# Performance work log

Measured on AMD Instinct MI355X. Metric: run time of the kernel, lower is better.

## Reference

```python
import jax, jax.numpy as jnp
import numpy as np

N = 64
D_MODEL = 512
L_MAX = 2048
BATCH = 8
DT_MIN, DT_MAX = 1e-3, 1e-1


def _make_s4_buffers(n):
    r = np.arange(1, n + 1, dtype=np.float64)
    # hippo[i,j] = sqrt(2(i+1)+1)*sqrt(2(j+1)+1) if i>j, (i+1)+1 on diag, else 0
    hippo = np.where(r[:, None] > r[None, :],
                     np.sqrt(2 * r[:, None] + 1.0) * np.sqrt(2 * r[None, :] + 1.0),
                     0.0)
    hippo = hippo + np.diag(r + 1.0)
    nhippo = -hippo
    p = 0.5 * np.sqrt(2.0 * r + 1.0)
    q = 2.0 * p
    S = nhippo + p[:, None] * q[None, :]
    lmbda, V = np.linalg.eig(S)
    Vc = V.conj().T
    p = Vc @ p
    q = Vc @ q.conj()
    return (p.astype(np.complex64), q.astype(np.complex64), lmbda.astype(np.complex64))


def setup_inputs() -> dict:
    key = jax.random.key(0)
    ku, kb, kc, ks = jax.random.split(key, 4)
    u = jax.random.normal(ku, (BATCH, L_MAX, D_MODEL), dtype=jnp.float32)
    std = float(np.sqrt(2.0 / (N + D_MODEL)))  # xavier_normal for (n, d_model)
    B = jax.random.normal(kb, (D_MODEL, N), dtype=jnp.float32) * std
    Ct = jax.random.normal(kc, (D_MODEL, N), dtype=jnp.float32) * std
    D = jnp.ones((D_MODEL,), dtype=jnp.float32)
    scale = float(np.log(DT_MAX) - np.log(DT_MIN))
    log_step = jax.random.uniform(ks, (D_MODEL,), dtype=jnp.float32) * scale + float(np.log(DT_MIN))
    p, q, lmbda = _make_s4_buffers(N)
    omega_l = np.exp(2j * np.pi / L_MAX * np.arange(L_MAX)).astype(np.complex64)
    return {"u": u, "B": B, "Ct": Ct, "D": D, "log_step": log_step,
            "p": jnp.asarray(p), "q": jnp.asarray(q), "lmbda": jnp.asarray(lmbda),
            "omega_l": jnp.asarray(omega_l)}


def _s4_kernel(B, Ct, log_step, p, q, lmbda, omega_l):
    L = omega_l.shape[0]
    step = jnp.exp(log_step)                                   # [d]
    g = jnp.outer(2.0 / step, (1.0 - omega_l) / (1.0 + omega_l))  # [d, L] complex
    c = 2.0 / (1.0 + omega_l)                                  # [L]
    # shared Cauchy resolvent: 1/(g - lambda), [d, L, n]
    r = 1.0 / (g[:, :, None] - lmbda)
    a0 = jnp.conj(Ct)  # [d, n]
    a1 = jnp.conj(q)   # [n]
    k00 = jnp.einsum('dn,dln->dl', a0 * B, r)
    k01 = jnp.einsum('dn,dln->dl', a0 * p, r)
    k10 = jnp.einsum('dn,dln->dl', a1 * B, r)
    k11 = jnp.einsum('n,dln->dl', a1 * p, r)
    at_roots = c * (k00 - k01 * (1.0 / (1.0 + k11)) * k10)     # [d, L]
    Kf = jnp.fft.ifft(at_roots, n=L, axis=-1)
    order = (-jnp.arange(L)) % L                               # [0, L-1, ..., 1]
    return Kf[:, order].real                                   # [d, L] float32


def reference(u, B, Ct, D, log_step, p, q, lmbda, omega_l):
    L = u.shape[1]
    K = _s4_kernel(B, Ct, log_step, p, q, lmbda, omega_l)      # [d, L]
    # non-circular FFT convolution
    ud = jnp.fft.rfft(jnp.pad(u, ((0, 0), (0, L), (0, 0))), axis=1)   # [B, L+1, d]
    Kd = jnp.fft.rfft(jnp.pad(K, ((0, 0), (0, L))), axis=-1)          # [d, L+1]
    y = jnp.fft.irfft(ud.transpose(0, 2, 1) * Kd, axis=-1)[..., :L]   # [B, d, L]
    return y.transpose(0, 2, 1) + D[None, None, :] * u
```

## Files before the change

### kernel.cpp

```cpp
#include <hip/hip_runtime.h>
#include <hip/hip_bf16.h>

#define NT 256
#define R2f 0.70710678118654752f
#define CS1 0.92387953251128674f
#define SN1 0.38268343236508978f
#define PI2 6.2831853071795865f

__device__ __forceinline__ float2 cmulf(float2 a, float2 b) {
    return make_float2(a.x * b.x - a.y * b.y, a.x * b.y + a.y * b.x);
}
__device__ __forceinline__ float2 cadd(float2 a, float2 b) { return make_float2(a.x + b.x, a.y + b.y); }
__device__ __forceinline__ float2 csub(float2 a, float2 b) { return make_float2(a.x - b.x, a.y - b.y); }

template<bool INV>
__device__ __forceinline__ float2 tww(float2 v, float wx, float wy) {
    float sy = INV ? -wy : wy;
    return make_float2(v.x * wx - v.y * sy, v.x * sy + v.y * wx);
}
template<bool INV>
__device__ __forceinline__ float2 mul_mi(float2 v) {
    return INV ? make_float2(-v.y, v.x) : make_float2(v.y, -v.x);
}

template<bool INV>
__device__ __forceinline__ void dft4(float2& a, float2& b, float2& c, float2& d) {
    float2 t0 = cadd(a, c), t1 = csub(a, c);
    float2 t2 = cadd(b, d), t3 = csub(b, d);
    float2 jt3 = mul_mi<INV>(t3);
    a = cadd(t0, t2);
    c = csub(t0, t2);
    b = cadd(t1, jt3);
    d = csub(t1, jt3);
}

template<bool INV>
__device__ __forceinline__ void fft16_tail(float2 v[16]) {
    v[5]  = tww<INV>(v[5],  CS1, -SN1);
    v[9]  = tww<INV>(v[9],  R2f, -R2f);
    v[13] = tww<INV>(v[13], SN1, -CS1);
    v[6]  = tww<INV>(v[6],  R2f, -R2f);
    v[10] = mul_mi<INV>(v[10]);
    v[14] = tww<INV>(v[14], -R2f, -R2f);
    v[7]  = tww<INV>(v[7],  SN1, -CS1);
    v[11] = tww<INV>(v[11], -R2f, -R2f);
    v[15] = tww<INV>(v[15], -CS1,  SN1);
    dft4<INV>(v[0],  v[1],  v[2],  v[3]);
    dft4<INV>(v[4],  v[5],  v[6],  v[7]);
    dft4<INV>(v[8],  v[9],  v[10], v[11]);
    dft4<INV>(v[12], v[13], v[14], v[15]);
    float2 t;
    t = v[1];  v[1]  = v[4];  v[4]  = t;
    t = v[2];  v[2]  = v[8];  v[8]  = t;
    t = v[3];  v[3]  = v[12]; v[12] = t;
    t = v[6];  v[6]  = v[9];  v[9]  = t;
    t = v[7];  v[7]  = v[13]; v[13] = t;
    t = v[11]; v[11] = v[14]; v[14] = t;
}

template<bool INV>
__device__ __forceinline__ void fft16(float2 v[16]) {
    dft4<INV>(v[0], v[4], v[8],  v[12]);
    dft4<INV>(v[1], v[5], v[9],  v[13]);
    dft4<INV>(v[2], v[6], v[10], v[14]);
    dft4<INV>(v[3], v[7], v[11], v[15]);
    fft16_tail<INV>(v);
}

__device__ __forceinline__ void fft16_hz(float2 v[16]) {
    #pragma unroll
    for (int i = 0; i < 4; ++i) {
        float2 a = v[i], b = v[i + 4];
        float2 jb = make_float2(b.y, -b.x);
        v[i]      = cadd(a, b);
        v[i + 4]  = cadd(a, jb);
        v[i + 8]  = csub(a, b);
        v[i + 12] = csub(a, jb);
    }
    fft16_tail<false>(v);
}

template<bool INV>
__device__ __forceinline__ void twchain(float2 v[16], float ang) {
    float s, c;
    __sincosf(INV ? ang : -ang, &s, &c);
    float2 w = make_float2(c, s);
    float2 t = w;
    v[1] = cmulf(v[1], t);
    #pragma unroll
    for (int a = 2; a < 16; ++a) { t = cmulf(t, w); v[a] = cmulf(v[a], t); }
}

template<bool INV>
__device__ void fft4096(float2 v[16], float2* lds, int tid) {
    const int hi = tid >> 4, lo = tid & 15;
    if (!INV) {
        fft16_hz(v);
        twchain<false>(v, PI2 * (float)tid * (1.0f / 4096.0f));
        __syncthreads();
        #pragma unroll
        for (int a = 0; a < 16; ++a) lds[tid + 256 * a] = v[a];
        __syncthreads();
        #pragma unroll
        for (int m1 = 0; m1 < 16; ++m1) v[m1] = lds[(m1 * 16 + lo) + 256 * hi];
        fft16<false>(v);
        twchain<false>(v, PI2 * (float)lo * (1.0f / 256.0f));
        __syncthreads();
        #pragma unroll
        for (int b = 0; b < 16; ++b) { int e = lo + 16 * b + 256 * hi; lds[e ^ b] = v[b]; }
        __syncthreads();
        #pragma unroll
        for (int m0 = 0; m0 < 16; ++m0) { int e = m0 + 16 * lo + 256 * hi; v[m0] = lds[e ^ lo]; }
        fft16<false>(v);
    } else {
        fft16<true>(v);
        __syncthreads();
        #pragma unroll
        for (int m0 = 0; m0 < 16; ++m0) { int e = m0 + 16 * lo + 256 * hi; lds[e ^ lo] = v[m0]; }
        __syncthreads();
        #pragma unroll
        for (int b = 0; b < 16; ++b) { int e = lo + 16 * b + 256 * hi; v[b] = lds[e ^ b]; }
        twchain<true>(v, PI2 * (float)lo * (1.0f / 256.0f));
        fft16<true>(v);
        __syncthreads();
        #pragma unroll
        for (int m1 = 0; m1 < 16; ++m1) lds[(m1 * 16 + lo) + 256 * hi] = v[m1];
        __syncthreads();
        #pragma unroll
        for (int a = 0; a < 16; ++a) v[a] = lds[tid + 256 * a];
        twchain<true>(v, PI2 * (float)tid * (1.0f / 4096.0f));
        fft16<true>(v);
    }
}

__global__ __launch_bounds__(256) void cauchy_kernel(
    const float* __restrict__ Bmat, const float* __restrict__ Ct,
    const float* __restrict__ log_step,
    const float2* __restrict__ p, const float2* __restrict__ q,
    const float2* __restrict__ lmbda, const float2* __restrict__ omega,
    float2* __restrict__ at)
{
    __shared__ float4 wA[64];
    __shared__ float4 wB[64];
    const int tid = threadIdx.x;
    const int d = blockIdx.x >> 1;
    const int lbase = (blockIdx.x & 1) << 9;

    if (tid < 64) {
        float b  = Bmat[d * 64 + tid];
        float ct = Ct[d * 64 + tid];
        float2 pp = p[tid], qq = q[tid];
        float2 lam = lmbda[tid];
        wA[tid] = make_float4(lam.x, lam.y, ct * b, qq.x * pp.x + qq.y * pp.y);
        wB[tid] = make_float4(ct * pp.x, ct * pp.y, b * qq.x, b * qq.y);
    }
    __syncthreads();

    const float two_over_dt = 2.0f * __expf(-log_step[d]);
    float2* atd = at + ((size_t)d << 11);

    float gx[2], gy[2], ccx[2], ccy[2];
    float S00x[2], S00y[2], Sax[2], Say[2], Sbx[2], Sby[2];
    float Scx[2], Scy[2], Sdx[2], Sdy[2], S11x[2], S11y[2];

    #pragma unroll
    for (int il = 0; il < 2; ++il) {
        int l = lbase + tid + 256 * il;
        float2 om = omega[l];
        float dnx = 1.0f + om.x, dny = om.y;
        float id2 = __builtin_amdgcn_rcpf(dnx * dnx + dny * dny);
        float ivx = dnx * id2, ivy = -dny * id2;
        ccx[il] = 2.0f * ivx; ccy[il] = 2.0f * ivy;
        float nmx = 1.0f - om.x, nmy = -om.y;
        gx[il] = two_over_dt * (nmx * ivx - nmy * ivy);
        gy[il] = two_over_dt * (nmx * ivy + nmy * ivx);
        S00x[il] = 0.f; S00y[il] = 0.f; Sax[il] = 0.f; Say[il] = 0.f;
        Sbx[il] = 0.f; Sby[il] = 0.f; Scx[il] = 0.f; Scy[il] = 0.f;
        Sdx[il] = 0.f; Sdy[il] = 0.f; S11x[il] = 0.f; S11y[il] = 0.f;
    }

    #pragma unroll 4
    for (int n = 0; n < 64; ++n) {
        float4 A  = wA[n];
        float4 Bw = wB[n];
        #pragma unroll
        for (int il = 0; il < 2; ++il) {
            float dx  = gx[il] - A.x;
            float dy  = gy[il] - A.y;
            float ir  = __builtin_amdgcn_rcpf(fmaf(dx, dx, dy * dy));
            float rx  = dx * ir;
            float ry  = -dy * ir;
            S00x[il] = fmaf(A.z,  rx, S00x[il]); S00y[il] = fmaf(A.z,  ry, S00y[il]);
            S11x[il] = fmaf(A.w,  rx, S11x[il]); S11y[il] = fmaf(A.w,  ry, S11y[il]);
            Sax[il]  = fmaf(Bw.x, rx, Sax[il]);  Say[il]  = fmaf(Bw.x, ry, Say[il]);
            Sbx[il]  = fmaf(Bw.y, rx, Sbx[il]);  Sby[il]  = fmaf(Bw.y, ry, Sby[il]);
            Scx[il]  = fmaf(Bw.z, rx, Scx[il]);  Scy[il]  = fmaf(Bw.z, ry, Scy[il]);
            Sdx[il]  = fmaf(Bw.w, rx, Sdx[il]);  Sdy[il]  = fmaf(Bw.w, ry, Sdy[il]);
        }
    }

    #pragma unroll
    for (int il = 0; il < 2; ++il) {
        float k01x = Sax[il] - Sby[il], k01y = Say[il] + Sbx[il];
        float k10x = Scx[il] + Sdy[il], k10y = Scy[il] - Sdx[il];
        float ntx = k01x * k10x - k01y * k10y;
        float nty = k01x * k10y + k01y * k10x;
        float ox = 1.0f + S11x[il], oy = S11y[il];
        float oid = __builtin_amdgcn_rcpf(ox * ox + oy * oy);
        float tx = (ntx * ox + nty * oy) * oid;
        float ty = (nty * ox - ntx * oy) * oid;
        float inx = S00x[il] - tx, iny = S00y[il] - ty;
        int l = lbase + tid + 256 * il;
        float2 val = make_float2(ccx[il] * inx - ccy[il] * iny,
                                 ccx[il] * iny + ccy[il] * inx);
        atd[l] = val;
        if (l != 0) atd[2048 - l] = make_float2(val.x, -val.y);
    }

    if ((blockIdx.x & 1) && tid == 0) {
        float2 om = omega[1024];
        float dnx = 1.0f + om.x, dny = om.y;
        float id2 = __builtin_amdgcn_rcpf(dnx * dnx + dny * dny);
        float ivx = dnx * id2, ivy = -dny * id2;
        float cx = 2.0f * ivx, cy = 2.0f * ivy;
        float nmx = 1.0f - om.x, nmy = -om.y;
        float ggx = two_over_dt * (nmx * ivx - nmy * ivy);
        float ggy = two_over_dt * (nmx * ivy + nmy * ivx);
        float s00x = 0.f, s00y = 0.f, sax = 0.f, say = 0.f, sbx = 0.f, sby = 0.f;
        float scx = 0.f, scy = 0.f, sdx = 0.f, sdy = 0.f, s11x = 0.f, s11y = 0.f;
        for (int n = 0; n < 64; ++n) {
            float4 A  = wA[n];
            float4 Bw = wB[n];
            float dx  = ggx - A.x;
            float dy  = ggy - A.y;
            float ir  = __builtin_amdgcn_rcpf(fmaf(dx, dx, dy * dy));
            float rx  = dx * ir;
            float ry  = -dy * ir;
            s00x = fmaf(A.z,  rx, s00x); s00y = fmaf(A.z,  ry, s00y);
            s11x = fmaf(A.w,  rx, s11x); s11y = fmaf(A.w,  ry, s11y);
            sax  = fmaf(Bw.x, rx, sax);  say  = fmaf(Bw.x, ry, say);
            sbx  = fmaf(Bw.y, rx, sbx);  sby  = fmaf(Bw.y, ry, sby);
            scx  = fmaf(Bw.z, rx, scx);  scy  = fmaf(Bw.z, ry, scy);
            sdx  = fmaf(Bw.w, rx, sdx);  sdy  = fmaf(Bw.w, ry, sdy);
        }
        float k01x = sax - sby, k01y = say + sbx;
        float k10x = scx + sdy, k10y = scy - sdx;
        float ntx = k01x * k10x - k01y * k10y;
        float nty = k01x * k10y + k01y * k10x;
        float ox = 1.0f + s11x, oy = s11y;
        float oid = __builtin_amdgcn_rcpf(ox * ox + oy * oy);
        float tx = (ntx * ox + nty * oy) * oid;
        float ty = (nty * ox - ntx * oy) * oid;
        float inx = s00x - tx, iny = s00y - ty;
        atd[1024] = make_float2(cx * inx - cy * iny, cx * iny + cy * inx);
    }
}

__global__ __launch_bounds__(256) void khat_kernel(
    const float2* __restrict__ at, float2* __restrict__ Khat)
{
    __shared__ float2 lds[4096];
    const int tid = threadIdx.x;
    const int d = blockIdx.x;
    const int hi = tid >> 4, lo = tid & 15;
    float2 v[16];

    const float2* ap = at + ((size_t)d << 11);
    #pragma unroll
    for (int n2 = 0; n2 < 8; ++n2) v[n2] = ap[tid + 256 * n2];
    #pragma unroll
    for (int n2 = 8; n2 < 16; ++n2) v[n2] = make_float2(0.f, 0.f);

    fft4096<false>(v, lds, tid);

    float* ldsf = (float*)lds;
    __syncthreads();
    if (!(hi & 1)) {
        int a2 = hi >> 1;
        #pragma unroll
        for (int c = 0; c < 16; ++c) {
            int j = 128 * c + 8 * lo + a2;
            ldsf[j ^ ((j >> 5) & 3)] = v[c].x * (1.0f / (2048.0f * 4096.0f));
        }
    }
    __syncthreads();
    #pragma unroll
    for (int n2 = 0; n2 < 8; ++n2) {
        int j = tid + 256 * n2;
        v[n2] = make_float2(ldsf[j ^ ((j >> 5) & 3)], 0.f);
    }
    #pragma unroll
    for (int n2 = 8; n2 < 16; ++n2) v[n2] = make_float2(0.f, 0.f);

    fft4096<false>(v, lds, tid);

    float2* op = Khat + ((size_t)d << 12);
    #pragma unroll
    for (int c = 0; c < 16; ++c) op[c * 256 + tid] = v[c];
}

__global__ __launch_bounds__(256) void transpose_pack_kernel(
    const float* __restrict__ u, float2* __restrict__ z)
{
    __shared__ float2 tile[64][65];
    int blk = blockIdx.x;
    int lt  = blk & 31;
    int dt8 = (blk >> 5) & 7;
    int bp  = blk >> 8;
    const size_t ub0 = (size_t)(2 * bp) * 2048 * 512;
    const size_t ub1 = (size_t)(2 * bp + 1) * 2048 * 512;
    for (int r = 0; r < 16; ++r) {
        int idx = threadIdx.x + 256 * r;
        int row = idx >> 6;
        int col = idx & 63;
        size_t off = (size_t)(lt * 64 + row) * 512 + (dt8 * 64 + col);
        tile[col][row] = make_float2(u[ub0 + off], u[ub1 + off]);
    }
    __syncthreads();
    for (int r = 0; r < 16; ++r) {
        int idx = threadIdx.x + 256 * r;
        int row = idx >> 6;
        int col = idx & 63;
        z[((size_t)(bp * 512 + dt8 * 64 + row)) * 2048 + lt * 64 + col] = tile[row][col];
    }
}

__global__ __launch_bounds__(256) void conv_kernel(
    float2* __restrict__ z, const float2* __restrict__ Khat,
    const float* __restrict__ D)
{
    __shared__ float2 lds[4096];
    const int tid = threadIdx.x;
    const int d  = blockIdx.x & 511;
    const int bp = blockIdx.x >> 9;
    float2 v[16];
    float2 u0[8];

    float2* zr = z + ((size_t)(bp * 512 + d)) * 2048;
    #pragma unroll
    for (int n2 = 0; n2 < 8; ++n2) { u0[n2] = zr[tid + 256 * n2]; v[n2] = u0[n2]; }
    #pragma unroll
    for (int n2 = 8; n2 < 16; ++n2) v[n2] = make_float2(0.f, 0.f);

    fft4096<false>(v, lds, tid);

    const float2* kh = Khat + ((size_t)d << 12);
    #pragma unroll
    for (int c = 0; c < 16; ++c) v[c] = cmulf(v[c], kh[c * 256 + tid]);

    fft4096<true>(v, lds, tid);

    const float Dd = D[d];
    #pragma unroll
    for (int n2 = 0; n2 < 8; ++n2) {
        zr[tid + 256 * n2] =
            make_float2(v[n2].x + Dd * u0[n2].x, v[n2].y + Dd * u0[n2].y);
    }
}

__global__ __launch_bounds__(256) void untranspose_kernel(
    const float2* __restrict__ yz, float* __restrict__ out)
{
    __shared__ float2 tile[64][65];
    int blk = blockIdx.x;
    int lt  = blk & 31;
    int dt8 = (blk >> 5) & 7;
    int bp  = blk >> 8;
    for (int r = 0; r < 16; ++r) {
        int idx = threadIdx.x + 256 * r;
        int row = idx >> 6;
        int col = idx & 63;
        float2 vv = yz[((size_t)(bp * 512 + dt8 * 64 + row)) * 2048 + lt * 64 + col];
        tile[col][row] = vv;
    }
    __syncthreads();
    const size_t ub0 = (size_t)(2 * bp) * 2048 * 512;
    const size_t ub1 = (size_t)(2 * bp + 1) * 2048 * 512;
    for (int r = 0; r < 16; ++r) {
        int idx = threadIdx.x + 256 * r;
        int row = idx >> 6;
        int col = idx & 63;
        size_t off = (size_t)(lt * 64 + row) * 512 + (dt8 * 64 + col);
        float2 vv = tile[row][col];
        out[ub0 + off] = vv.x;
        out[ub1 + off] = vv.y;
    }
}

extern "C" void kernel_launch(void* const* d_in, const int* in_sizes, int n_in,
                              void* d_out, int out_size, void* d_ws, size_t ws_size,
                              hipStream_t stream) {
    (void)in_sizes; (void)n_in; (void)out_size; (void)ws_size;
    const float*  u   = (const float*)d_in[0];
    const float*  Bm  = (const float*)d_in[1];
    const float*  Ct  = (const float*)d_in[2];
    const float*  D   = (const float*)d_in[3];
    const float*  ls  = (const float*)d_in[4];
    const float2* p   = (const float2*)d_in[5];
    const float2* q   = (const float2*)d_in[6];
    const float2* lm  = (const float2*)d_in[7];
    const float2* om  = (const float2*)d_in[8];
    float* out = (float*)d_out;

    float2* Khat = (float2*)d_ws;
    float2* z    = (float2*)((char*)d_ws + (size_t)512 * 4096 * 8);
    float2* at   = z;

    hipLaunchKernelGGL(cauchy_kernel, dim3(1024), dim3(256), 0, stream,
                       Bm, Ct, ls, p, q, lm, om, at);
    hipLaunchKernelGGL(khat_kernel, dim3(512), dim3(256), 0, stream, at, Khat);
    hipLaunchKernelGGL(transpose_pack_kernel, dim3(1024), dim3(256), 0, stream, u, z);
    hipLaunchKernelGGL(conv_kernel, dim3(2048), dim3(256), 0, stream, z, Khat, D);
    hipLaunchKernelGGL(untranspose_kernel, dim3(1024), dim3(256), 0, stream, z, out);
}
```

Baseline: 93.16 us.

## Fuse Cauchy evaluation and input transpose into one role-split launch

Merges the compute-bound Cauchy kernel and the memory-bound transpose/pack kernel into a single launch where even blocks transpose and odd blocks compute Cauchy. The Cauchy output moves to a separate workspace region so it no longer aliases z. The aim is to overlap ALU-heavy and bandwidth-heavy work and drop one launch. It needs extra workspace, falls back to the old path if that is missing, and the fused kernel carries the larger shared memory footprint for every block.

```diff
diff --git a/kernel.cpp b/kernel.cpp
--- a/kernel.cpp
+++ b/kernel.cpp
@@ -133,18 +133,15 @@
     }
 }
 
-__global__ __launch_bounds__(256) void cauchy_kernel(
+__device__ __forceinline__ void cauchy_body(
     const float* __restrict__ Bmat, const float* __restrict__ Ct,
     const float* __restrict__ log_step,
     const float2* __restrict__ p, const float2* __restrict__ q,
     const float2* __restrict__ lmbda, const float2* __restrict__ omega,
-    float2* __restrict__ at)
-{
-    __shared__ float4 wA[64];
-    __shared__ float4 wB[64];
-    const int tid = threadIdx.x;
-    const int d = blockIdx.x >> 1;
-    const int lbase = (blockIdx.x & 1) << 9;
+    float2* __restrict__ at, int sub, int tid, float4* wA, float4* wB)
+{
+    const int d = sub >> 1;
+    const int lbase = (sub & 1) << 9;
 
     if (tid < 64) {
         float b  = Bmat[d * 64 + tid];
@@ -217,7 +214,7 @@
         if (l != 0) atd[2048 - l] = make_float2(val.x, -val.y);
     }
 
-    if ((blockIdx.x & 1) && tid == 0) {
+    if ((sub & 1) && tid == 0) {
         float2 om = omega[1024];
         float dnx = 1.0f + om.x, dny = om.y;
         float id2 = __builtin_amdgcn_rcpf(dnx * dnx + dny * dny);
@@ -256,6 +253,73 @@
     }
 }
 
+__device__ __forceinline__ void transpose_body(
+    const float* __restrict__ u, float2* __restrict__ z,
+    int sub, int tid, float2 (*tile)[65])
+{
+    int lt  = sub & 31;
+    int dt8 = (sub >> 5) & 7;
+    int bp  = sub >> 8;
+    const size_t ub0 = (size_t)(2 * bp) * 2048 * 512;
+    const size_t ub1 = (size_t)(2 * bp + 1) * 2048 * 512;
+    for (int r = 0; r < 16; ++r) {
+        int idx = tid + 256 * r;
+        int row = idx >> 6;
+        int col = idx & 63;
+        size_t off = (size_t)(lt * 64 + row) * 512 + (dt8 * 64 + col);
+        tile[col][row] = make_float2(u[ub0 + off], u[ub1 + off]);
+    }
+    __syncthreads();
+    for (int r = 0; r < 16; ++r) {
+        int idx = tid + 256 * r;
+        int row = idx >> 6;
+        int col = idx & 63;
+        z[((size_t)(bp * 512 + dt8 * 64 + row)) * 2048 + lt * 64 + col] = tile[row][col];
+    }
+}
+
+__global__ __launch_bounds__(256) void fused_cauchy_transpose_kernel(
+    const float* __restrict__ Bmat, const float* __restrict__ Ct,
+    const float* __restrict__ log_step,
+    const float2* __restrict__ p, const float2* __restrict__ q,
+    const float2* __restrict__ lmbda, const float2* __restrict__ omega,
+    float2* __restrict__ at,
+    const float* __restrict__ u, float2* __restrict__ z)
+{
+    __shared__ float2 tile[64][65];
+    __shared__ float4 wA[64];
+    __shared__ float4 wB[64];
+    const int tid = threadIdx.x;
+    const int role = blockIdx.x & 1;
+    const int sub  = blockIdx.x >> 1;
+
+    if (role == 0) {
+        transpose_body(u, z, sub, tid, tile);
+    } else {
+        cauchy_body(Bmat, Ct, log_step, p, q, lmbda, omega, at, sub, tid, wA, wB);
+    }
+}
+
+__global__ __launch_bounds__(256) void cauchy_kernel(
+    const float* __restrict__ Bmat, const float* __restrict__ Ct,
+    const float* __restrict__ log_step,
+    const float2* __restrict__ p, const float2* __restrict__ q,
+    const float2* __restrict__ lmbda, const float2* __restrict__ omega,
+    float2* __restrict__ at)
+{
+    __shared__ float4 wA[64];
+    __shared__ float4 wB[64];
+    cauchy_body(Bmat, Ct, log_step, p, q, lmbda, omega, at,
+                blockIdx.x, threadIdx.x, wA, wB);
+}
+
+__global__ __launch_bounds__(256) void transpose_pack_kernel(
+    const float* __restrict__ u, float2* __restrict__ z)
+{
+    __shared__ float2 tile[64][65];
+    transpose_body(u, z, blockIdx.x, threadIdx.x, tile);
+}
+
 __global__ __launch_bounds__(256) void khat_kernel(
     const float2* __restrict__ at, float2* __restrict__ Khat)
 {
@@ -297,32 +361,6 @@
     float2* op = Khat + ((size_t)d << 12);
     #pragma unroll
     for (int c = 0; c < 16; ++c) op[c * 256 + tid] = v[c];
-}
-
-__global__ __launch_bounds__(256) void transpose_pack_kernel(
-    const float* __restrict__ u, float2* __restrict__ z)
-{
-    __shared__ float2 tile[64][65];
-    int blk = blockIdx.x;
-    int lt  = blk & 31;
-    int dt8 = (blk >> 5) & 7;
-    int bp  = blk >> 8;
-    const size_t ub0 = (size_t)(2 * bp) * 2048 * 512;
-    const size_t ub1 = (size_t)(2 * bp + 1) * 2048 * 512;
-    for (int r = 0; r < 16; ++r) {
-        int idx = threadIdx.x + 256 * r;
-        int row = idx >> 6;
-        int col = idx & 63;
-        size_t off = (size_t)(lt * 64 + row) * 512 + (dt8 * 64 + col);
-        tile[col][row] = make_float2(u[ub0 + off], u[ub1 + off]);
-    }
-    __syncthreads();
-    for (int r = 0; r < 16; ++r) {
-        int idx = threadIdx.x + 256 * r;
-        int row = idx >> 6;
-        int col = idx & 63;
-        z[((size_t)(bp * 512 + dt8 * 64 + row)) * 2048 + lt * 64 + col] = tile[row][col];
-    }
 }
 
 __global__ __launch_bounds__(256) void conv_kernel(
@@ -390,7 +428,7 @@
 extern "C" void kernel_launch(void* const* d_in, const int* in_sizes, int n_in,
                               void* d_out, int out_size, void* d_ws, size_t ws_size,
                               hipStream_t stream) {
-    (void)in_sizes; (void)n_in; (void)out_size; (void)ws_size;
+    (void)in_sizes; (void)n_in; (void)out_size;
     const float*  u   = (const float*)d_in[0];
     const float*  Bm  = (const float*)d_in[1];
     const float*  Ct  = (const float*)d_in[2];
@@ -402,14 +440,25 @@
     const float2* om  = (const float2*)d_in[8];
     float* out = (float*)d_out;
 
+    const size_t KHAT_B = (size_t)512 * 4096 * sizeof(float2);
+    const size_t Z_B    = (size_t)2048 * 2048 * sizeof(float2);
+    const size_t AT_B   = (size_t)512 * 2048 * sizeof(float2);
+
     float2* Khat = (float2*)d_ws;
-    float2* z    = (float2*)((char*)d_ws + (size_t)512 * 4096 * 8);
-    float2* at   = z;
-
-    hipLaunchKernelGGL(cauchy_kernel, dim3(1024), dim3(256), 0, stream,
-                       Bm, Ct, ls, p, q, lm, om, at);
-    hipLaunchKernelGGL(khat_kernel, dim3(512), dim3(256), 0, stream, at, Khat);
-    hipLaunchKernelGGL(transpose_pack_kernel, dim3(1024), dim3(256), 0, stream, u, z);
+    float2* z    = (float2*)((char*)d_ws + KHAT_B);
+
+    if (ws_size >= KHAT_B + Z_B + AT_B) {
+        float2* at = (float2*)((char*)d_ws + KHAT_B + Z_B);
+        hipLaunchKernelGGL(fused_cauchy_transpose_kernel, dim3(2048), dim3(256), 0, stream,
+                           Bm, Ct, ls, p, q, lm, om, at, u, z);
+        hipLaunchKernelGGL(khat_kernel, dim3(512), dim3(256), 0, stream, at, Khat);
+    } else {
+        float2* at = z;
+        hipLaunchKernelGGL(cauchy_kernel, dim3(1024), dim3(256), 0, stream,
+                           Bm, Ct, ls, p, q, lm, om, at);
+        hipLaunchKernelGGL(khat_kernel, dim3(512), dim3(256), 0, stream, at, Khat);
+        hipLaunchKernelGGL(transpose_pack_kernel, dim3(1024), dim3(256), 0, stream, u, z);
+    }
     hipLaunchKernelGGL(conv_kernel, dim3(2048), dim3(256), 0, stream, z, Khat, D);
     hipLaunchKernelGGL(untranspose_kernel, dim3(1024), dim3(256), 0, stream, z, out);
 }
```

New measurement: 96.63 us. 1.04x slower.
